# Kernel tuning notes

Hardware: AMD Instinct MI355X
Metric: run time of the kernel (lower is better)

The kernel has to match this reference:

```python
import jax, jax.numpy as jnp
import numpy as np

N, E, F, H, C, K = 100000, 1600000, 512, 256, 64, 10
EPS = 1e-5  # BatchNorm1d default eps


def setup_inputs() -> dict:
    key = jax.random.key(0)
    ks = jax.random.split(key, 8)
    x = jax.random.normal(ks[0], (N, F), jnp.float32)
    # edge list with no self-loops (gcn_norm adds the self-loops itself)
    src = jax.random.randint(ks[1], (E,), 0, N)
    off = jax.random.randint(ks[2], (E,), 1, N)
    dst = (src + off) % N
    edge_index = jnp.stack([src, dst])
    s = lambda k, sh: jax.random.normal(k, sh, jnp.float32) * 0.02
    W0 = s(ks[3], (F, H)); b0 = jnp.zeros((H,), jnp.float32)
    g0 = jnp.ones((H,), jnp.float32); be0 = jnp.zeros((H,), jnp.float32)
    W1 = s(ks[4], (H, H)); b1 = jnp.zeros((H,), jnp.float32)
    g1 = jnp.ones((H,), jnp.float32); be1 = jnp.zeros((H,), jnp.float32)
    W2 = s(ks[5], (H, C)); b2 = jnp.zeros((C,), jnp.float32)
    proj_w = s(ks[6], (C, 1)); proj_b = jnp.zeros((1,), jnp.float32)
    return dict(x=x, W0=W0, b0=b0, g0=g0, be0=be0, W1=W1, b1=b1, g1=g1,
                be1=be1, W2=W2, b2=b2, proj_w=proj_w, proj_b=proj_b,
                edge_index=edge_index)


def _batchnorm(h, gamma, beta):
    # training-mode BN over the node (batch) axis, biased variance like torch
    mu = h.mean(0)
    var = h.var(0)
    return gamma * (h - mu) * jax.lax.rsqrt(var + EPS) + beta


def _prop(x, edge_index, proj_w, proj_b):
    n, c = x.shape
    loop = jnp.arange(n, dtype=edge_index.dtype)
    row = jnp.concatenate([edge_index[0], loop])  # message sources (x_j)
    col = jnp.concatenate([edge_index[1], loop])  # aggregation targets
    w = jnp.ones(row.shape, x.dtype)
    deg = jax.ops.segment_sum(w, col, num_segments=n)
    dis = jnp.where(deg > 0, jax.lax.rsqrt(jnp.maximum(deg, 1.0)) * (deg > 0), 0.0)
    dis = jnp.where(deg > 0, deg ** -0.5, 0.0)
    norm = dis[row] * dis[col]  # symmetric GCN normalization per edge

    def hop(xk, _):
        msgs = norm[:, None] * xk[row]               # gather + scale  [E+N, C]
        xk = jax.ops.segment_sum(msgs, col, num_segments=n)  # scatter-add
        return xk, xk

    _, hops = jax.lax.scan(hop, x, None, length=K)   # [K, N, C]
    pps = jnp.concatenate([x[None], hops], axis=0).transpose(1, 0, 2)  # [N, K+1, C]
    score = jax.nn.sigmoid(pps @ proj_w + proj_b)[..., 0]  # [N, K+1]
    return jnp.einsum('nk,nkc->nc', score, pps)      # [N, C]


def reference(x, W0, b0, g0, be0, W1, b1, g1, be1, W2, b2, proj_w, proj_b,
              edge_index):
    h = jax.nn.relu(_batchnorm(x @ W0 + b0, g0, be0))   # dropout is identity (eval)
    h = jax.nn.relu(_batchnorm(h @ W1 + b1, g1, be1))
    h = h @ W2 + b2                                     # [N, C] logits
    out = _prop(h, edge_index, proj_w, proj_b)
    return jax.nn.log_softmax(out, axis=1)
```

## Files before the change

kernel.cpp:

```cpp
#include <hip/hip_runtime.h>
#include <hip/hip_bf16.h>
#include <math.h>

#define NN 100000
#define FF 512
#define HH 256
#define CC 64
#define KHOPS 10
#define BN_EPS 1e-5f

typedef __bf16 bf16x8 __attribute__((ext_vector_type(8)));
typedef float f32x4 __attribute__((ext_vector_type(4)));
typedef unsigned short ushort8v __attribute__((ext_vector_type(8)));

__device__ __forceinline__ unsigned short f2bf(float f) {
    __bf16 b = (__bf16)f;
    return __builtin_bit_cast(unsigned short, b);
}
__device__ __forceinline__ float bf2f(unsigned short h) {
    unsigned u = ((unsigned)h) << 16;
    return __builtin_bit_cast(float, u);
}

__global__ void k_zero(float* p, int n) {
    int i = blockIdx.x * blockDim.x + threadIdx.x;
    if (i < n) p[i] = 0.f;
}

__global__ void k_deg_init(int* deg, int n) {
    int i = blockIdx.x * blockDim.x + threadIdx.x;
    if (i < n) deg[i] = 1;
}

__global__ void k_deg_count(const int* __restrict__ dst, int e, int* deg) {
    for (int i = blockIdx.x * blockDim.x + threadIdx.x; i < e; i += gridDim.x * blockDim.x)
        atomicAdd(&deg[dst[i]], 1);
}

__global__ void k_dis(const int* __restrict__ deg, float* dis, int n) {
    int i = blockIdx.x * blockDim.x + threadIdx.x;
    if (i < n) dis[i] = rsqrtf((float)deg[i]);
}

#define SCAN_B 1024
#define SCAN_NB ((NN + SCAN_B - 1) / SCAN_B)

__global__ void k_scan1(const int* __restrict__ deg, int* __restrict__ part, int n) {
    __shared__ int ls[SCAN_B];
    int i = blockIdx.x * SCAN_B + threadIdx.x;
    ls[threadIdx.x] = (i < n) ? deg[i] - 1 : 0;
    __syncthreads();
    for (int d = SCAN_B / 2; d > 0; d >>= 1) {
        if (threadIdx.x < d) ls[threadIdx.x] += ls[threadIdx.x + d];
        __syncthreads();
    }
    if (threadIdx.x == 0) part[blockIdx.x] = ls[0];
}

__global__ void k_scan2(int* part, int* offs_last, int nb) {
    if (threadIdx.x == 0) {
        int run = 0;
        for (int b = 0; b < nb; b++) { int v = part[b]; part[b] = run; run += v; }
        offs_last[0] = run;
    }
}

__global__ void k_scan3(const int* __restrict__ deg, const int* __restrict__ part,
                        int* __restrict__ offs, int* __restrict__ cur, int n) {
    __shared__ int ls[SCAN_B];
    int i = blockIdx.x * SCAN_B + threadIdx.x;
    int v = (i < n) ? deg[i] - 1 : 0;
    ls[threadIdx.x] = v;
    __syncthreads();
    for (int d = 1; d < SCAN_B; d <<= 1) {
        int t = (threadIdx.x >= d) ? ls[threadIdx.x - d] : 0;
        __syncthreads();
        ls[threadIdx.x] += t;
        __syncthreads();
    }
    if (i < n) {
        int ex = part[blockIdx.x] + ls[threadIdx.x] - v;
        offs[i] = ex;
        cur[i] = ex;
    }
}

__global__ void k_fill(const int* __restrict__ src, const int* __restrict__ dst, int e,
                       const float* __restrict__ dis, int* cursor,
                       int* __restrict__ csrc, float* __restrict__ cw) {
    for (int i = blockIdx.x * blockDim.x + threadIdx.x; i < e; i += gridDim.x * blockDim.x) {
        int d = dst[i];
        int s = src[i];
        int p = atomicAdd(&cursor[d], 1);
        csrc[p] = s;
        cw[p] = dis[s] * dis[d];
    }
}

__global__ void k_wt(const float* __restrict__ W, unsigned short* __restrict__ Wt,
                     int K, int N) {
    int i = blockIdx.x * blockDim.x + threadIdx.x;
    if (i < K * N) {
        int n = i / K;
        int k = i - n * K;
        Wt[i] = f2bf(W[(size_t)k * N + n]);
    }
}

template <int AF32, int BN_, int FUSEBN, int STATS>
__global__ __launch_bounds__(256) void k_gemm_mfma(
    const void* __restrict__ Av, const unsigned short* __restrict__ Bt,
    const float* __restrict__ bias, unsigned short* __restrict__ Cb,
    const float* __restrict__ bnscale, const float* __restrict__ bnshift,
    float* __restrict__ sum, float* __restrict__ sumsq,
    int M, int K, int Nd) {
    constexpr int NREP = BN_ / 32;
    constexpr int BSTEP = BN_ / 64;
    __shared__ unsigned short Asb[2][128 * 32];
    __shared__ unsigned short Bsb[2][BN_ * 32];
    const int tid = threadIdx.x;
    const int lane = tid & 63;
    const int wid = tid >> 6;
    const int wrow = wid >> 1, wcol = wid & 1;
    const int row_base = blockIdx.y * 128;
    const int col_base = blockIdx.x * BN_;

    const float* Af = (const float*)Av;
    const unsigned short* Ab = (const unsigned short*)Av;

    f32x4 acc[4][NREP];
#pragma unroll
    for (int m = 0; m < 4; m++)
#pragma unroll
        for (int n = 0; n < NREP; n++)
#pragma unroll
            for (int j = 0; j < 4; j++) acc[m][n][j] = 0.f;

    float4 aF[4];
    ushort8v aB[2];
    float4 scv0, scv1, shv0, shv1;
    ushort8v bR[BSTEP];

    auto issue_loads = [&](int kt) {
#pragma unroll
        for (int i = 0; i < 2; ++i) {
            int e = tid + i * 256;
            int row = e >> 2;
            int grow = row_base + row;
            int kc = kt + (e & 3) * 8;
            if (AF32) {
                if (grow < M) {
                    const float* p = Af + (size_t)grow * K + kc;
                    aF[2 * i] = *(const float4*)p;
                    aF[2 * i + 1] = *(const float4*)(p + 4);
                } else {
                    aF[2 * i] = make_float4(0.f, 0.f, 0.f, 0.f);
                    aF[2 * i + 1] = make_float4(0.f, 0.f, 0.f, 0.f);
                }
            } else {
                ushort8v z = {0, 0, 0, 0, 0, 0, 0, 0};
                aB[i] = (grow < M) ? *(const ushort8v*)(Ab + (size_t)grow * K + kc) : z;
            }
        }
        if (FUSEBN) {
            int kc = kt + (tid & 3) * 8;
            scv0 = *(const float4*)(bnscale + kc);
            scv1 = *(const float4*)(bnscale + kc + 4);
            shv0 = *(const float4*)(bnshift + kc);
            shv1 = *(const float4*)(bnshift + kc + 4);
        }
#pragma unroll
        for (int i = 0; i < BSTEP; ++i) {
            int e = tid + i * 256;
            int nn = e >> 2, c = e & 3;
            bR[i] = *(const ushort8v*)(Bt + (size_t)(col_base + nn) * K + kt + c * 8);
        }
    };

    auto commit = [&](int buf) {
#pragma unroll
        for (int i = 0; i < 2; ++i) {
            int e = tid + i * 256;
            ushort8v v;
            if (AF32) {
                float4 f0 = aF[2 * i], f1 = aF[2 * i + 1];
                v[0] = f2bf(f0.x); v[1] = f2bf(f0.y); v[2] = f2bf(f0.z); v[3] = f2bf(f0.w);
                v[4] = f2bf(f1.x); v[5] = f2bf(f1.y); v[6] = f2bf(f1.z); v[7] = f2bf(f1.w);
            } else if (FUSEBN) {
                ushort8v r = aB[i];
                v[0] = f2bf(fmaxf(bf2f(r[0]) * scv0.x + shv0.x, 0.f));
                v[1] = f2bf(fmaxf(bf2f(r[1]) * scv0.y + shv0.y, 0.f));
                v[2] = f2bf(fmaxf(bf2f(r[2]) * scv0.z + shv0.z, 0.f));
                v[3] = f2bf(fmaxf(bf2f(r[3]) * scv0.w + shv0.w, 0.f));
                v[4] = f2bf(fmaxf(bf2f(r[4]) * scv1.x + shv1.x, 0.f));
                v[5] = f2bf(fmaxf(bf2f(r[5]) * scv1.y + shv1.y, 0.f));
                v[6] = f2bf(fmaxf(bf2f(r[6]) * scv1.z + shv1.z, 0.f));
                v[7] = f2bf(fmaxf(bf2f(r[7]) * scv1.w + shv1.w, 0.f));
            } else {
                v = aB[i];
            }
            *(ushort8v*)(Asb[buf] + e * 8) = v;
        }
#pragma unroll
        for (int i = 0; i < BSTEP; ++i) {
            int e = tid + i * 256;
            *(ushort8v*)(Bsb[buf] + e * 8) = bR[i];
        }
    };

    const int nt = K / 32;
    issue_loads(0);
    commit(0);
    __syncthreads();

    for (int t = 0; t < nt; ++t) {
        int cur = t & 1;
        if (t + 1 < nt) issue_loads((t + 1) * 32);
        bf16x8 af[4], bfr[NREP];
#pragma unroll
        for (int m = 0; m < 4; ++m)
            af[m] = *(const bf16x8*)(Asb[cur] + (wrow * 64 + m * 16 + (lane & 15)) * 32 + (lane >> 4) * 8);
#pragma unroll
        for (int n = 0; n < NREP; ++n)
            bfr[n] = *(const bf16x8*)(Bsb[cur] + (wcol * (BN_ / 2) + n * 16 + (lane & 15)) * 32 + (lane >> 4) * 8);
#pragma unroll
        for (int m = 0; m < 4; ++m)
#pragma unroll
            for (int n = 0; n < NREP; ++n)
                acc[m][n] = __builtin_amdgcn_mfma_f32_16x16x32_bf16(af[m], bfr[n], acc[m][n], 0, 0, 0);
        if (t + 1 < nt) commit(1 - cur);
        __syncthreads();
    }

    const int lc = lane & 15;
    const int lr = (lane >> 4) * 4;
#pragma unroll
    for (int m = 0; m < 4; ++m) {
        int gr0 = row_base + wrow * 64 + m * 16 + lr;
#pragma unroll
        for (int n = 0; n < NREP; ++n) {
            int gc = col_base + wcol * (BN_ / 2) + n * 16 + lc;
            float bb = bias[gc];
#pragma unroll
            for (int j = 0; j < 4; ++j) {
                int gr = gr0 + j;
                if (gr < M) Cb[(size_t)gr * Nd + gc] = f2bf(acc[m][n][j] + bb);
            }
        }
    }
    if (STATS) {
#pragma unroll
        for (int n = 0; n < NREP; ++n) {
            int gc = col_base + wcol * (BN_ / 2) + n * 16 + lc;
            float bb = bias[gc];
            float s = 0.f, s2 = 0.f;
#pragma unroll
            for (int m = 0; m < 4; ++m) {
                int gr0 = row_base + wrow * 64 + m * 16 + lr;
#pragma unroll
                for (int j = 0; j < 4; ++j) {
                    if (gr0 + j < M) {
                        float v = acc[m][n][j] + bb;
                        s += v;
                        s2 += v * v;
                    }
                }
            }
            s += __shfl_xor(s, 16); s += __shfl_xor(s, 32);
            s2 += __shfl_xor(s2, 16); s2 += __shfl_xor(s2, 32);
            if ((lane >> 4) == 0) {
                atomicAdd(&sum[gc], s);
                atomicAdd(&sumsq[gc], s2);
            }
        }
    }
}

__global__ void k_bnfin(const float* __restrict__ sum, const float* __restrict__ sq,
                        const float* __restrict__ g, const float* __restrict__ be,
                        float* scale, float* shift) {
    int c = threadIdx.x;
    float mu = sum[c] * (1.f / NN);
    float var = sq[c] * (1.f / NN) - mu * mu;
    float sc = g[c] * rsqrtf(var + BN_EPS);
    scale[c] = sc;
    shift[c] = be[c] - mu * sc;
}

__global__ void k_hop(const unsigned short* __restrict__ xin,
                      unsigned short* __restrict__ xout,
                      const int* __restrict__ offs, const int* __restrict__ csrc,
                      const float* __restrict__ cw, const float* __restrict__ dis,
                      int n) {
    int wid = (int)((blockIdx.x * (size_t)blockDim.x + threadIdx.x) >> 6);
    if (wid >= n) return;
    int lane = threadIdx.x & 63;
    int hf = lane >> 5;
    int l = lane & 31;
    const unsigned* x32 = (const unsigned*)xin;
    unsigned* o32 = (unsigned*)xout;
    float y0 = 0.f, y1 = 0.f;
    if (hf == 0) {
        float dn = dis[wid];
        float w = dn * dn;
        unsigned sv = x32[(size_t)wid * 32 + l];
        y0 = w * bf2f((unsigned short)(sv & 0xFFFF));
        y1 = w * bf2f((unsigned short)(sv >> 16));
    }
    int p0 = offs[wid], p1 = offs[wid + 1];
    int p = p0 + hf;
    for (; p + 2 < p1; p += 4) {
        int sA = csrc[p], sB = csrc[p + 2];
        float wA = cw[p], wB = cw[p + 2];
        unsigned vA = x32[(size_t)sA * 32 + l];
        unsigned vB = x32[(size_t)sB * 32 + l];
        y0 += wA * bf2f((unsigned short)(vA & 0xFFFF));
        y1 += wA * bf2f((unsigned short)(vA >> 16));
        y0 += wB * bf2f((unsigned short)(vB & 0xFFFF));
        y1 += wB * bf2f((unsigned short)(vB >> 16));
    }
    for (; p < p1; p += 2) {
        int s = csrc[p];
        float w = cw[p];
        unsigned v = x32[(size_t)s * 32 + l];
        y0 += w * bf2f((unsigned short)(v & 0xFFFF));
        y1 += w * bf2f((unsigned short)(v >> 16));
    }
    y0 += __shfl_xor(y0, 32);
    y1 += __shfl_xor(y1, 32);
    if (hf == 0)
        o32[(size_t)wid * 32 + l] = ((unsigned)f2bf(y1) << 16) | (unsigned)f2bf(y0);
}

struct XPack { const unsigned short* p[KHOPS + 1]; };

__global__ void k_finprop(XPack xp, const float* __restrict__ pw,
                          const float* __restrict__ pbp, float* __restrict__ out, int n) {
    int gw = (int)((blockIdx.x * (size_t)blockDim.x + threadIdx.x) >> 6);
    int lane = threadIdx.x & 63;
    int hf = lane >> 5;
    int l = lane & 31;
    int node = gw * 2 + hf;
    if (node >= n) return;
    float pw0 = pw[2 * l], pw1 = pw[2 * l + 1];
    float pb0 = pbp[0];
    float o0 = 0.f, o1 = 0.f;
#pragma unroll
    for (int k = 0; k <= KHOPS; k++) {
        unsigned v = ((const unsigned*)xp.p[k])[(size_t)node * 32 + l];
        float v0 = bf2f((unsigned short)(v & 0xFFFF));
        float v1 = bf2f((unsigned short)(v >> 16));
        float d = v0 * pw0 + v1 * pw1;
#pragma unroll
        for (int m = 16; m >= 1; m >>= 1) d += __shfl_xor(d, m);
        float s = 1.f / (1.f + expf(-(d + pb0)));
        o0 += s * v0;
        o1 += s * v1;
    }
    float mx = fmaxf(o0, o1);
#pragma unroll
    for (int m = 16; m >= 1; m >>= 1) mx = fmaxf(mx, __shfl_xor(mx, m));
    float e = expf(o0 - mx) + expf(o1 - mx);
#pragma unroll
    for (int m = 16; m >= 1; m >>= 1) e += __shfl_xor(e, m);
    float lg = mx + logf(e);
    float2 r = make_float2(o0 - lg, o1 - lg);
    *(float2*)(out + (size_t)node * 64 + 2 * l) = r;
}

extern "C" void kernel_launch(void* const* d_in, const int* in_sizes, int n_in,
                              void* d_out, int out_size, void* d_ws, size_t ws_size,
                              hipStream_t stream) {
    const float* x  = (const float*)d_in[0];
    const float* W0 = (const float*)d_in[1];
    const float* b0 = (const float*)d_in[2];
    const float* g0 = (const float*)d_in[3];
    const float* be0 = (const float*)d_in[4];
    const float* W1 = (const float*)d_in[5];
    const float* b1 = (const float*)d_in[6];
    const float* g1 = (const float*)d_in[7];
    const float* be1 = (const float*)d_in[8];
    const float* W2 = (const float*)d_in[9];
    const float* b2 = (const float*)d_in[10];
    const float* pw = (const float*)d_in[11];
    const float* pb = (const float*)d_in[12];
    const int* ei = (const int*)d_in[13];
    const int E = in_sizes[13] / 2;
    const int* esrc = ei;
    const int* edst = ei + E;

    char* ws = (char*)d_ws;
    const size_t XKB = (size_t)NN * CC * 2;
    unsigned short* h0b = (unsigned short*)(ws + 0);
    unsigned short* h1b = (unsigned short*)(ws + 51200000);
    unsigned short* xk[KHOPS + 1];
    xk[0] = (unsigned short*)(ws + 0);
    xk[5] = (unsigned short*)(ws + XKB);
    xk[6] = (unsigned short*)(ws + 2 * XKB);
    xk[7] = (unsigned short*)(ws + 3 * XKB);
    xk[1] = (unsigned short*)(ws + 51200000);
    xk[2] = (unsigned short*)(ws + 51200000 + XKB);
    xk[3] = (unsigned short*)(ws + 51200000 + 2 * XKB);
    xk[4] = (unsigned short*)(ws + 51200000 + 3 * XKB);
    xk[8] = (unsigned short*)(ws + 102400000);
    xk[9] = (unsigned short*)(ws + 115200000);
    xk[10] = (unsigned short*)(ws + 128000000);

    int*   deg  = (int*)  (ws + 140800000);
    float* dis  = (float*)(ws + 141200000);
    int*   offs = (int*)  (ws + 141600000);
    int*   cur  = (int*)  (ws + 142000064);
    int*   csrc = (int*)  (ws + 142400064);
    float* cw   = (float*)(ws + 148800064);
    float* stats = (float*)(ws + 155200064);
    int*   part = (int*)  (ws + 155208256);
    unsigned short* W0t = (unsigned short*)(ws + 155209280);
    unsigned short* W1t = (unsigned short*)(ws + 155471424);
    unsigned short* W2t = (unsigned short*)(ws + 155602496);

    float* sum0 = stats,        *sq0 = stats + 256;
    float* sum1 = stats + 512,  *sq1 = stats + 768;
    float* scale0 = stats + 1024, *shift0 = stats + 1280;
    float* scale1 = stats + 1536, *shift1 = stats + 1792;

    float* out = (float*)d_out;

    const int TPB = 256;
    int ngrid = (NN + TPB - 1) / TPB;
    int egrid = (E + TPB - 1) / TPB;
    int wgrid = (NN * 64 + TPB - 1) / TPB;
    int wgrid2 = (((NN + 1) / 2) * 64 + TPB - 1) / TPB;
    int mtiles = (NN + 127) / 128;

    k_zero<<<2, 1024, 0, stream>>>(stats, 2048);
    k_deg_init<<<ngrid, TPB, 0, stream>>>(deg, NN);
    k_deg_count<<<egrid, TPB, 0, stream>>>(edst, E, deg);
    k_dis<<<ngrid, TPB, 0, stream>>>(deg, dis, NN);
    k_scan1<<<SCAN_NB, SCAN_B, 0, stream>>>(deg, part, NN);
    k_scan2<<<1, 64, 0, stream>>>(part, offs + NN, SCAN_NB);
    k_scan3<<<SCAN_NB, SCAN_B, 0, stream>>>(deg, part, offs, cur, NN);
    k_fill<<<egrid, TPB, 0, stream>>>(esrc, edst, E, dis, cur, csrc, cw);

    k_wt<<<(FF * HH + TPB - 1) / TPB, TPB, 0, stream>>>(W0, W0t, FF, HH);
    k_wt<<<(HH * HH + TPB - 1) / TPB, TPB, 0, stream>>>(W1, W1t, HH, HH);
    k_wt<<<(HH * CC + TPB - 1) / TPB, TPB, 0, stream>>>(W2, W2t, HH, CC);

    k_gemm_mfma<1, 128, 0, 1><<<dim3(HH / 128, mtiles), 256, 0, stream>>>(
        x, W0t, b0, h0b, nullptr, nullptr, sum0, sq0, NN, FF, HH);
    k_bnfin<<<1, 256, 0, stream>>>(sum0, sq0, g0, be0, scale0, shift0);

    k_gemm_mfma<0, 128, 1, 1><<<dim3(HH / 128, mtiles), 256, 0, stream>>>(
        h0b, W1t, b1, h1b, scale0, shift0, sum1, sq1, NN, HH, HH);
    k_bnfin<<<1, 256, 0, stream>>>(sum1, sq1, g1, be1, scale1, shift1);

    k_gemm_mfma<0, 64, 1, 0><<<dim3(1, mtiles), 256, 0, stream>>>(
        h1b, W2t, b2, xk[0], scale1, shift1, nullptr, nullptr, NN, HH, CC);

    for (int k = 0; k < KHOPS; k++)
        k_hop<<<wgrid, TPB, 0, stream>>>(xk[k], xk[k + 1], offs, csrc, cw, dis, NN);

    XPack xp;
    for (int k = 0; k <= KHOPS; k++) xp.p[k] = xk[k];
    k_finprop<<<wgrid2, TPB, 0, stream>>>(xp, pw, pb, out, NN);
}
```

Measured before the change: 1.086 ms.

## Use direct global-to-LDS loads in GEMM, split BN apply, widen hop gathers

The GEMM now loads A and B tiles straight into LDS with global_load_lds, using an XOR-swizzled layout. It drops the register-staged double buffering and converts fp32 A to bf16 when reading from LDS. Because of that, the BN scale/shift/ReLU fused into the next GEMM's A-load moves out into a separate in-place elementwise kernel, which costs an extra read and write pass over each hidden activation. The propagation hop kernel now gives 16 lanes per edge with 8-byte loads, processing four edges in parallel per wave, and reduces across quarters with shuffles.

```diff
diff --git a/kernel.cpp b/kernel.cpp
--- a/kernel.cpp
+++ b/kernel.cpp
@@ -20,6 +20,12 @@
 __device__ __forceinline__ float bf2f(unsigned short h) {
     unsigned u = ((unsigned)h) << 16;
     return __builtin_bit_cast(float, u);
+}
+
+typedef __attribute__((address_space(1))) const void g_void;
+typedef __attribute__((address_space(3))) void l_void;
+__device__ __forceinline__ void gl2lds16(const void* g, void* l) {
+    __builtin_amdgcn_global_load_lds((g_void*)g, (l_void*)l, 16, 0, 0);
 }
 
 __global__ void k_zero(float* p, int n) {
@@ -107,26 +113,26 @@
     }
 }
 
-template <int AF32, int BN_, int FUSEBN, int STATS>
+template <int AF32, int BN_, int STATS>
 __global__ __launch_bounds__(256) void k_gemm_mfma(
     const void* __restrict__ Av, const unsigned short* __restrict__ Bt,
     const float* __restrict__ bias, unsigned short* __restrict__ Cb,
-    const float* __restrict__ bnscale, const float* __restrict__ bnshift,
     float* __restrict__ sum, float* __restrict__ sumsq,
     int M, int K, int Nd) {
     constexpr int NREP = BN_ / 32;
-    constexpr int BSTEP = BN_ / 64;
-    __shared__ unsigned short Asb[2][128 * 32];
-    __shared__ unsigned short Bsb[2][BN_ * 32];
+    constexpr int ACH = AF32 ? 8 : 4;
+    constexpr int AOPS = AF32 ? 4 : 2;
+    constexpr int ASZ = AF32 ? 16384 : 8192;
+    __shared__ __align__(16) unsigned char Asb[ASZ];
+    __shared__ __align__(16) unsigned char Bsb[BN_ * 64];
     const int tid = threadIdx.x;
     const int lane = tid & 63;
     const int wid = tid >> 6;
     const int wrow = wid >> 1, wcol = wid & 1;
     const int row_base = blockIdx.y * 128;
     const int col_base = blockIdx.x * BN_;
-
-    const float* Af = (const float*)Av;
-    const unsigned short* Ab = (const unsigned short*)Av;
+    const unsigned char* Abase = (const unsigned char*)Av;
+    const size_t arowb = (size_t)K * (AF32 ? 4 : 2);
 
     f32x4 acc[4][NREP];
 #pragma unroll
@@ -136,99 +142,58 @@
 #pragma unroll
             for (int j = 0; j < 4; j++) acc[m][n][j] = 0.f;
 
-    float4 aF[4];
-    ushort8v aB[2];
-    float4 scv0, scv1, shv0, shv1;
-    ushort8v bR[BSTEP];
-
-    auto issue_loads = [&](int kt) {
-#pragma unroll
-        for (int i = 0; i < 2; ++i) {
-            int e = tid + i * 256;
-            int row = e >> 2;
-            int grow = row_base + row;
-            int kc = kt + (e & 3) * 8;
+    for (int kt = 0; kt < K; kt += 32) {
+#pragma unroll
+        for (int i = 0; i < AOPS; ++i) {
+            int e = i * 256 + tid;
+            int r = e / ACH;
+            int c = e % ACH;
+            int cs = AF32 ? (c ^ (r & 7)) : (c ^ ((r >> 1) & 3));
+            int grow = row_base + r;
+            if (grow > M - 1) grow = M - 1;
+            const void* g = Abase + (size_t)grow * arowb + (size_t)kt * (AF32 ? 4 : 2) + (cs << 4);
+            gl2lds16(g, Asb + e * 16);
+        }
+#pragma unroll
+        for (int i = 0; i < BN_ / 64; ++i) {
+            int e = i * 256 + tid;
+            int r = e >> 2, c = e & 3;
+            int cs = c ^ ((r >> 1) & 3);
+            const void* g = (const unsigned char*)Bt + (size_t)(col_base + r) * (K * 2) +
+                            (size_t)kt * 2 + (cs << 4);
+            gl2lds16(g, Bsb + e * 16);
+        }
+        __syncthreads();
+
+        bf16x8 af[4], bfr[NREP];
+#pragma unroll
+        for (int m = 0; m < 4; ++m) {
+            int r = wrow * 64 + m * 16 + (lane & 15);
             if (AF32) {
-                if (grow < M) {
-                    const float* p = Af + (size_t)grow * K + kc;
-                    aF[2 * i] = *(const float4*)p;
-                    aF[2 * i + 1] = *(const float4*)(p + 4);
-                } else {
-                    aF[2 * i] = make_float4(0.f, 0.f, 0.f, 0.f);
-                    aF[2 * i + 1] = make_float4(0.f, 0.f, 0.f, 0.f);
-                }
+                int x7 = r & 7;
+                int q2 = (lane >> 4) * 2;
+                f32x4 f0 = *(const f32x4*)(Asb + r * 128 + ((q2 ^ x7) << 4));
+                f32x4 f1 = *(const f32x4*)(Asb + r * 128 + (((q2 + 1) ^ x7) << 4));
+                bf16x8 a;
+                a[0] = (__bf16)f0[0]; a[1] = (__bf16)f0[1]; a[2] = (__bf16)f0[2]; a[3] = (__bf16)f0[3];
+                a[4] = (__bf16)f1[0]; a[5] = (__bf16)f1[1]; a[6] = (__bf16)f1[2]; a[7] = (__bf16)f1[3];
+                af[m] = a;
             } else {
-                ushort8v z = {0, 0, 0, 0, 0, 0, 0, 0};
-                aB[i] = (grow < M) ? *(const ushort8v*)(Ab + (size_t)grow * K + kc) : z;
+                int cs = (lane >> 4) ^ ((r >> 1) & 3);
+                af[m] = *(const bf16x8*)(Asb + r * 64 + (cs << 4));
             }
         }
-        if (FUSEBN) {
-            int kc = kt + (tid & 3) * 8;
-            scv0 = *(const float4*)(bnscale + kc);
-            scv1 = *(const float4*)(bnscale + kc + 4);
-            shv0 = *(const float4*)(bnshift + kc);
-            shv1 = *(const float4*)(bnshift + kc + 4);
-        }
-#pragma unroll
-        for (int i = 0; i < BSTEP; ++i) {
-            int e = tid + i * 256;
-            int nn = e >> 2, c = e & 3;
-            bR[i] = *(const ushort8v*)(Bt + (size_t)(col_base + nn) * K + kt + c * 8);
-        }
-    };
-
-    auto commit = [&](int buf) {
-#pragma unroll
-        for (int i = 0; i < 2; ++i) {
-            int e = tid + i * 256;
-            ushort8v v;
-            if (AF32) {
-                float4 f0 = aF[2 * i], f1 = aF[2 * i + 1];
-                v[0] = f2bf(f0.x); v[1] = f2bf(f0.y); v[2] = f2bf(f0.z); v[3] = f2bf(f0.w);
-                v[4] = f2bf(f1.x); v[5] = f2bf(f1.y); v[6] = f2bf(f1.z); v[7] = f2bf(f1.w);
-            } else if (FUSEBN) {
-                ushort8v r = aB[i];
-                v[0] = f2bf(fmaxf(bf2f(r[0]) * scv0.x + shv0.x, 0.f));
-                v[1] = f2bf(fmaxf(bf2f(r[1]) * scv0.y + shv0.y, 0.f));
-                v[2] = f2bf(fmaxf(bf2f(r[2]) * scv0.z + shv0.z, 0.f));
-                v[3] = f2bf(fmaxf(bf2f(r[3]) * scv0.w + shv0.w, 0.f));
-                v[4] = f2bf(fmaxf(bf2f(r[4]) * scv1.x + shv1.x, 0.f));
-                v[5] = f2bf(fmaxf(bf2f(r[5]) * scv1.y + shv1.y, 0.f));
-                v[6] = f2bf(fmaxf(bf2f(r[6]) * scv1.z + shv1.z, 0.f));
-                v[7] = f2bf(fmaxf(bf2f(r[7]) * scv1.w + shv1.w, 0.f));
-            } else {
-                v = aB[i];
-            }
-            *(ushort8v*)(Asb[buf] + e * 8) = v;
-        }
-#pragma unroll
-        for (int i = 0; i < BSTEP; ++i) {
-            int e = tid + i * 256;
-            *(ushort8v*)(Bsb[buf] + e * 8) = bR[i];
-        }
-    };
-
-    const int nt = K / 32;
-    issue_loads(0);
-    commit(0);
-    __syncthreads();
-
-    for (int t = 0; t < nt; ++t) {
-        int cur = t & 1;
-        if (t + 1 < nt) issue_loads((t + 1) * 32);
-        bf16x8 af[4], bfr[NREP];
-#pragma unroll
-        for (int m = 0; m < 4; ++m)
-            af[m] = *(const bf16x8*)(Asb[cur] + (wrow * 64 + m * 16 + (lane & 15)) * 32 + (lane >> 4) * 8);
-#pragma unroll
-        for (int n = 0; n < NREP; ++n)
-            bfr[n] = *(const bf16x8*)(Bsb[cur] + (wcol * (BN_ / 2) + n * 16 + (lane & 15)) * 32 + (lane >> 4) * 8);
+#pragma unroll
+        for (int n = 0; n < NREP; ++n) {
+            int r = wcol * (BN_ / 2) + n * 16 + (lane & 15);
+            int cs = (lane >> 4) ^ ((r >> 1) & 3);
+            bfr[n] = *(const bf16x8*)(Bsb + r * 64 + (cs << 4));
+        }
 #pragma unroll
         for (int m = 0; m < 4; ++m)
 #pragma unroll
             for (int n = 0; n < NREP; ++n)
                 acc[m][n] = __builtin_amdgcn_mfma_f32_16x16x32_bf16(af[m], bfr[n], acc[m][n], 0, 0, 0);
-        if (t + 1 < nt) commit(1 - cur);
         __syncthreads();
     }
 
@@ -287,6 +252,26 @@
     shift[c] = be[c] - mu * sc;
 }
 
+__global__ void k_bnapply(unsigned short* __restrict__ h, const float* __restrict__ scale,
+                          const float* __restrict__ shift, int n) {
+    int total = n * 32;
+    for (int idx = blockIdx.x * blockDim.x + threadIdx.x; idx < total;
+         idx += gridDim.x * blockDim.x) {
+        int c8 = (idx & 31) * 8;
+        ushort8v v = *(ushort8v*)(h + (size_t)idx * 8);
+        f32x4 s0 = *(const f32x4*)(scale + c8);
+        f32x4 s1 = *(const f32x4*)(scale + c8 + 4);
+        f32x4 h0 = *(const f32x4*)(shift + c8);
+        f32x4 h1 = *(const f32x4*)(shift + c8 + 4);
+#pragma unroll
+        for (int j = 0; j < 4; j++) {
+            v[j] = f2bf(fmaxf(bf2f(v[j]) * s0[j] + h0[j], 0.f));
+            v[j + 4] = f2bf(fmaxf(bf2f(v[j + 4]) * s1[j] + h1[j], 0.f));
+        }
+        *(ushort8v*)(h + (size_t)idx * 8) = v;
+    }
+}
+
 __global__ void k_hop(const unsigned short* __restrict__ xin,
                       unsigned short* __restrict__ xout,
                       const int* __restrict__ offs, const int* __restrict__ csrc,
@@ -295,41 +280,57 @@
     int wid = (int)((blockIdx.x * (size_t)blockDim.x + threadIdx.x) >> 6);
     if (wid >= n) return;
     int lane = threadIdx.x & 63;
-    int hf = lane >> 5;
-    int l = lane & 31;
-    const unsigned* x32 = (const unsigned*)xin;
-    unsigned* o32 = (unsigned*)xout;
-    float y0 = 0.f, y1 = 0.f;
-    if (hf == 0) {
+    int q = lane >> 4;
+    int l = lane & 15;
+    const uint2* x8 = (const uint2*)xin;
+    float y0 = 0.f, y1 = 0.f, y2 = 0.f, y3 = 0.f;
+    if (q == 0) {
         float dn = dis[wid];
         float w = dn * dn;
-        unsigned sv = x32[(size_t)wid * 32 + l];
-        y0 = w * bf2f((unsigned short)(sv & 0xFFFF));
-        y1 = w * bf2f((unsigned short)(sv >> 16));
+        uint2 v = x8[(size_t)wid * 16 + l];
+        y0 = w * bf2f((unsigned short)(v.x & 0xFFFF));
+        y1 = w * bf2f((unsigned short)(v.x >> 16));
+        y2 = w * bf2f((unsigned short)(v.y & 0xFFFF));
+        y3 = w * bf2f((unsigned short)(v.y >> 16));
     }
     int p0 = offs[wid], p1 = offs[wid + 1];
-    int p = p0 + hf;
-    for (; p + 2 < p1; p += 4) {
-        int sA = csrc[p], sB = csrc[p + 2];
-        float wA = cw[p], wB = cw[p + 2];
-        unsigned vA = x32[(size_t)sA * 32 + l];
-        unsigned vB = x32[(size_t)sB * 32 + l];
-        y0 += wA * bf2f((unsigned short)(vA & 0xFFFF));
-        y1 += wA * bf2f((unsigned short)(vA >> 16));
-        y0 += wB * bf2f((unsigned short)(vB & 0xFFFF));
-        y1 += wB * bf2f((unsigned short)(vB >> 16));
-    }
-    for (; p < p1; p += 2) {
+    int p = p0 + q;
+    for (; p + 4 < p1; p += 8) {
+        int sA = csrc[p], sB = csrc[p + 4];
+        float wA = cw[p], wB = cw[p + 4];
+        uint2 vA = x8[(size_t)sA * 16 + l];
+        uint2 vB = x8[(size_t)sB * 16 + l];
+        y0 += wA * bf2f((unsigned short)(vA.x & 0xFFFF));
+        y1 += wA * bf2f((unsigned short)(vA.x >> 16));
+        y2 += wA * bf2f((unsigned short)(vA.y & 0xFFFF));
+        y3 += wA * bf2f((unsigned short)(vA.y >> 16));
+        y0 += wB * bf2f((unsigned short)(vB.x & 0xFFFF));
+        y1 += wB * bf2f((unsigned short)(vB.x >> 16));
+        y2 += wB * bf2f((unsigned short)(vB.y & 0xFFFF));
+        y3 += wB * bf2f((unsigned short)(vB.y >> 16));
+    }
+    for (; p < p1; p += 4) {
         int s = csrc[p];
         float w = cw[p];
-        unsigned v = x32[(size_t)s * 32 + l];
-        y0 += w * bf2f((unsigned short)(v & 0xFFFF));
-        y1 += w * bf2f((unsigned short)(v >> 16));
-    }
-    y0 += __shfl_xor(y0, 32);
-    y1 += __shfl_xor(y1, 32);
-    if (hf == 0)
-        o32[(size_t)wid * 32 + l] = ((unsigned)f2bf(y1) << 16) | (unsigned)f2bf(y0);
+        uint2 v = x8[(size_t)s * 16 + l];
+        y0 += w * bf2f((unsigned short)(v.x & 0xFFFF));
+        y1 += w * bf2f((unsigned short)(v.x >> 16));
+        y2 += w * bf2f((unsigned short)(v.y & 0xFFFF));
+        y3 += w * bf2f((unsigned short)(v.y >> 16));
+    }
+#pragma unroll
+    for (int m = 16; m <= 32; m <<= 1) {
+        y0 += __shfl_xor(y0, m);
+        y1 += __shfl_xor(y1, m);
+        y2 += __shfl_xor(y2, m);
+        y3 += __shfl_xor(y3, m);
+    }
+    if (q == 0) {
+        uint2 r;
+        r.x = ((unsigned)f2bf(y1) << 16) | (unsigned)f2bf(y0);
+        r.y = ((unsigned)f2bf(y3) << 16) | (unsigned)f2bf(y2);
+        ((uint2*)xout)[(size_t)wid * 16 + l] = r;
+    }
 }
 
 struct XPack { const unsigned short* p[KHOPS + 1]; };
@@ -445,16 +446,18 @@
     k_wt<<<(HH * HH + TPB - 1) / TPB, TPB, 0, stream>>>(W1, W1t, HH, HH);
     k_wt<<<(HH * CC + TPB - 1) / TPB, TPB, 0, stream>>>(W2, W2t, HH, CC);
 
-    k_gemm_mfma<1, 128, 0, 1><<<dim3(HH / 128, mtiles), 256, 0, stream>>>(
-        x, W0t, b0, h0b, nullptr, nullptr, sum0, sq0, NN, FF, HH);
+    k_gemm_mfma<1, 128, 1><<<dim3(HH / 128, mtiles), 256, 0, stream>>>(
+        x, W0t, b0, h0b, sum0, sq0, NN, FF, HH);
     k_bnfin<<<1, 256, 0, stream>>>(sum0, sq0, g0, be0, scale0, shift0);
-
-    k_gemm_mfma<0, 128, 1, 1><<<dim3(HH / 128, mtiles), 256, 0, stream>>>(
-        h0b, W1t, b1, h1b, scale0, shift0, sum1, sq1, NN, HH, HH);
+    k_bnapply<<<2048, TPB, 0, stream>>>(h0b, scale0, shift0, NN);
+
+    k_gemm_mfma<0, 128, 1><<<dim3(HH / 128, mtiles), 256, 0, stream>>>(
+        h0b, W1t, b1, h1b, sum1, sq1, NN, HH, HH);
     k_bnfin<<<1, 256, 0, stream>>>(sum1, sq1, g1, be1, scale1, shift1);
-
-    k_gemm_mfma<0, 64, 1, 0><<<dim3(1, mtiles), 256, 0, stream>>>(
-        h1b, W2t, b2, xk[0], scale1, shift1, nullptr, nullptr, NN, HH, CC);
+    k_bnapply<<<2048, TPB, 0, stream>>>(h1b, scale1, shift1, NN);
+
+    k_gemm_mfma<0, 64, 0><<<dim3(1, mtiles), 256, 0, stream>>>(
+        h1b, W2t, b2, xk[0], nullptr, nullptr, NN, HH, CC);
 
     for (int k = 0; k < KHOPS; k++)
         k_hop<<<wgrid, TPB, 0, stream>>>(xk[k], xk[k + 1], offs, csrc, cw, dis, NN);
```

New measurement: 954.4 us. -12.1%, faster.
